# Kernel tuning notes

Measured on AMD Instinct MI355X. Metric: run time of the kernel, lower is better.

Reference implementation:

```python
import jax, jax.numpy as jnp
import numpy as np

N_NODES = 50000
N_EDGES = 800000
N_GRAPHS = 64
IN_C, HID, OUT_C = 128, 96, 96
EPS = 1e-5


def gcn_conv(x, W, b, src, dst, n_nodes):
    # PyG GCNConv: linear -> symmetric-normalized aggregation with self-loops
    h = x @ W  # [N, C]
    deg = jax.ops.segment_sum(jnp.ones(src.shape[0], h.dtype), dst, num_segments=n_nodes) + 1.0  # +1 self-loop
    dinv = jax.lax.rsqrt(deg)  # deg >= 1, no inf
    norm = dinv[src] * dinv[dst]  # [E]
    agg = jax.ops.segment_sum(h[src] * norm[:, None], dst, num_segments=n_nodes)
    agg = agg + h * (dinv * dinv)[:, None]  # self-loop contribution
    return agg + b


def graph_norm(x, w, b, alpha, batch, n_graphs):
    # PyG GraphNorm: per-graph mean (scaled by learnable alpha) and variance
    cnt = jax.ops.segment_sum(jnp.ones(x.shape[0], x.dtype), batch, num_segments=n_graphs)[:, None]
    mean = jax.ops.segment_sum(x, batch, num_segments=n_graphs) / cnt
    xc = x - alpha * mean[batch]
    var = jax.ops.segment_sum(xc * xc, batch, num_segments=n_graphs) / cnt
    return w * xc * jax.lax.rsqrt(var[batch] + EPS) + b


def setup_inputs() -> dict:
    key = jax.random.key(0)
    ks = jax.random.split(key, 8)
    x = jax.random.normal(ks[0], (N_NODES, IN_C), jnp.float32)
    edge_index = jax.random.randint(ks[1], (2, N_EDGES), 0, N_NODES, jnp.int64)
    batch = jnp.sort(jax.random.randint(ks[2], (N_NODES,), 0, N_GRAPHS, jnp.int64))
    s1 = 1.0 / np.sqrt(IN_C)
    s2 = 1.0 / np.sqrt(HID)
    return {
        "x": x,
        "edge_index": edge_index,
        "batch": batch,
        "W1": jax.random.uniform(ks[3], (IN_C, HID), jnp.float32, -s1, s1),
        "b1": jnp.zeros((HID,), jnp.float32),
        "gn1_w": jnp.ones((HID,), jnp.float32),
        "gn1_b": jnp.zeros((HID,), jnp.float32),
        "gn1_a": jnp.ones((HID,), jnp.float32),
        "W2": jax.random.uniform(ks[4], (HID, OUT_C), jnp.float32, -s2, s2),
        "b2": jnp.zeros((OUT_C,), jnp.float32),
        "gn2_w": jnp.ones((OUT_C,), jnp.float32),
        "gn2_b": jnp.zeros((OUT_C,), jnp.float32),
        "gn2_a": jnp.ones((OUT_C,), jnp.float32),
    }


def reference(x, edge_index, batch, W1, b1, gn1_w, gn1_b, gn1_a, W2, b2, gn2_w, gn2_b, gn2_a):
    src, dst = edge_index[0], edge_index[1]
    h = gcn_conv(x, W1, b1, src, dst, N_NODES)
    h = graph_norm(h, gn1_w, gn1_b, gn1_a, batch, N_GRAPHS)
    h = jax.nn.relu(h)  # dropout = identity in eval mode
    h = gcn_conv(h, W2, b2, src, dst, N_NODES)
    h = graph_norm(h, gn2_w, gn2_b, gn2_a, batch, N_GRAPHS)
    h = jax.nn.relu(h)
    return h
```

## Files before the change

kernel.cpp:

```cpp
#include <hip/hip_runtime.h>
#include <hip/hip_bf16.h>

#define N_NODES 50000
#define N_EDGES 800000
#define N_GRAPHS 64
#define IN_C 128
#define HID 96
#define SLICES 8
#define NBUCK 196
#define NCHK 200
#define EPC 4000

typedef short s16x8 __attribute__((ext_vector_type(8)));
typedef float f32x4 __attribute__((ext_vector_type(4)));

__device__ inline unsigned short f2bf(float f) {
    union { __hip_bfloat16 b; unsigned short u; } cv;
    cv.b = __float2bfloat16(f);
    return cv.u;
}
__device__ inline float bf2f(unsigned short u) { return __uint_as_float((unsigned int)u << 16); }
__device__ inline float bf_lo(unsigned int u) { return __uint_as_float(u << 16); }
__device__ inline float bf_hi(unsigned int u) { return __uint_as_float(u & 0xffff0000u); }
__device__ inline unsigned int pack2(float lo, float hi) {
    return (unsigned)f2bf(lo) | ((unsigned)f2bf(hi) << 16);
}
__device__ inline void acc8(float* a, uint4 r) {
    a[0] += bf_lo(r.x); a[1] += bf_hi(r.x);
    a[2] += bf_lo(r.y); a[3] += bf_hi(r.y);
    a[4] += bf_lo(r.z); a[5] += bf_hi(r.z);
    a[6] += bf_lo(r.w); a[7] += bf_hi(r.w);
}


__global__ __launch_bounds__(256)
void p1_hist(const int* __restrict__ dst, int* __restrict__ chunkHist,
             const int* __restrict__ batch, int* __restrict__ gstart, int* __restrict__ gend) {
    __shared__ int h[NBUCK];
    int c = blockIdx.x, t = threadIdx.x;
    for (int i = t; i < NBUCK; i += 256) h[i] = 0;
    __syncthreads();
    int base = c * EPC;
    for (int i = t; i < EPC; i += 256)
        atomicAdd(&h[dst[base + i] >> 8], 1);
    __syncthreads();
    for (int i = t; i < NBUCK; i += 256) chunkHist[c * NBUCK + i] = h[i];

    int gi = c * 256 + t;
    if (gi < N_NODES) {
        int g = batch[gi];
        if (gi == 0) {
            gstart[g] = 0;
        } else {
            int gp = batch[gi - 1];
            if (gp != g) { gstart[g] = gi; gend[gp] = gi - 1; }
        }
        if (gi == N_NODES - 1) gend[g] = N_NODES - 1;
    }
}

__global__ __launch_bounds__(256)
void p2a_scan(const int* __restrict__ chunkHist, int* __restrict__ offTabRel,
              int* __restrict__ bucketTot) {
    __shared__ int sh[256];
    __shared__ int hv[256];
    int b = blockIdx.x, t = threadIdx.x;
    int v = (t < NCHK) ? chunkHist[t * NBUCK + b] : 0;
    hv[t] = v;
    sh[t] = v;
    __syncthreads();
    for (int off = 1; off < 256; off <<= 1) {
        int x = (t >= off) ? sh[t - off] : 0;
        __syncthreads();
        sh[t] += x;
        __syncthreads();
    }
    if (t < NCHK) offTabRel[t * NBUCK + b] = sh[t] - hv[t];
    if (t == 255) bucketTot[b] = sh[255];
}

__global__ __launch_bounds__(256)
void p2b_base(const int* __restrict__ bucketTot, int* __restrict__ bucketBase,
              int* __restrict__ rowstart) {
    __shared__ int sh[256];
    int t = threadIdx.x;
    int v = (t < NBUCK) ? bucketTot[t] : 0;
    sh[t] = v;
    __syncthreads();
    for (int off = 1; off < 256; off <<= 1) {
        int x = (t >= off) ? sh[t - off] : 0;
        __syncthreads();
        sh[t] += x;
        __syncthreads();
    }
    if (t < NBUCK) bucketBase[t] = sh[t] - v;
    if (t == 0) { bucketBase[NBUCK] = N_EDGES; rowstart[N_NODES] = N_EDGES; }
}

__global__ __launch_bounds__(256)
void p3_place(const int* __restrict__ src, const int* __restrict__ dst,
              const int* __restrict__ offTabRel, const int* __restrict__ bucketBase,
              unsigned int* __restrict__ epacked) {
    __shared__ int cur[NBUCK];
    int c = blockIdx.x, t = threadIdx.x;
    for (int i = t; i < NBUCK; i += 256)
        cur[i] = bucketBase[i] + offTabRel[c * NBUCK + i];
    __syncthreads();
    int base = c * EPC;
    for (int i = t; i < EPC; i += 256) {
        int d = dst[base + i];
        int s = src[base + i];
        int pos = atomicAdd(&cur[d >> 8], 1);
        epacked[pos] = ((unsigned)(d & 255) << 16) | (unsigned)s;
    }
}

__global__ __launch_bounds__(256)
void p4_fine(const unsigned int* __restrict__ epacked, const int* __restrict__ bucketBase,
             int* __restrict__ rowstart, float* __restrict__ dinv,
             unsigned short* __restrict__ e_src16) {
    __shared__ int h[256];
    __shared__ int rs[256];
    __shared__ unsigned short sorted[8192];
    int b = blockIdx.x, t = threadIdx.x;
    int s0 = bucketBase[b], len = bucketBase[b + 1] - s0;
    h[t] = 0;
    __syncthreads();
    for (int i = t; i < len; i += 256)
        atomicAdd(&h[(epacked[s0 + i] >> 16) & 255], 1);
    __syncthreads();
    int deg = h[t];
    rs[t] = deg;
    __syncthreads();
    for (int off = 1; off < 256; off <<= 1) {
        int x = (t >= off) ? rs[t - off] : 0;
        __syncthreads();
        rs[t] += x;
        __syncthreads();
    }
    int myrow = rs[t] - deg;
    int node = b * 256 + t;
    if (node < N_NODES) {
        rowstart[node] = s0 + myrow;
        dinv[node] = rsqrtf((float)deg + 1.0f);
    }
    __syncthreads();
    h[t] = myrow;
    __syncthreads();
    for (int i = t; i < len; i += 256) {
        unsigned int p = epacked[s0 + i];
        int pos = atomicAdd(&h[(p >> 16) & 255], 1);
        sorted[pos] = (unsigned short)(p & 0xffffu);
    }
    __syncthreads();
    for (int i = t; i < len; i += 256) e_src16[s0 + i] = sorted[i];
}

template <int K, bool PRENORM>
__global__ __launch_bounds__(256)
void gemm_mfma(const void* __restrict__ Xv, const float* __restrict__ W,
               const float* __restrict__ dinv, const int* __restrict__ batch,
               const float* __restrict__ gA, const float* __restrict__ gB,
               unsigned short* __restrict__ Hp) {
    constexpr int KP = K + 8;
    constexpr int KS = K / 32;
    __shared__ unsigned short Wt[96 * KP];
    int tid = threadIdx.x;
    for (int idx = tid; idx < K * 96; idx += 256) {
        int k = idx / 96, c = idx - k * 96;
        Wt[c * KP + k] = f2bf(W[idx]);
    }
    __syncthreads();

    const int lane = tid & 63;
    const int quad = lane >> 4;
    const int l16 = lane & 15;

    s16x8 Bf[6][KS];
#pragma unroll
    for (int t = 0; t < 6; ++t)
#pragma unroll
        for (int s = 0; s < KS; ++s)
            Bf[t][s] = *(const s16x8*)&Wt[(t * 16 + l16) * KP + s * 32 + quad * 8];

    int gw = blockIdx.x * 4 + (tid >> 6);
    int nw = gridDim.x * 4;
    for (int tile = gw; tile < N_NODES / 16; tile += nw) {
        int n0 = tile * 16;
        int row = n0 + l16;
        s16x8 Af[KS];
        if (!PRENORM) {
            const float* Xr = (const float*)Xv + (size_t)row * K;
#pragma unroll
            for (int s = 0; s < KS; ++s) {
                int k0 = s * 32 + quad * 8;
                float4 u = *(const float4*)(Xr + k0);
                float4 v = *(const float4*)(Xr + k0 + 4);
                s16x8 a;
                a[0] = (short)f2bf(u.x); a[1] = (short)f2bf(u.y);
                a[2] = (short)f2bf(u.z); a[3] = (short)f2bf(u.w);
                a[4] = (short)f2bf(v.x); a[5] = (short)f2bf(v.y);
                a[6] = (short)f2bf(v.z); a[7] = (short)f2bf(v.w);
                Af[s] = a;
            }
        } else {
            const unsigned short* Xr = (const unsigned short*)Xv + (size_t)row * HID;
            int g = batch[row];
            const float* ga = gA + g * HID;
            const float* gb = gB + g * HID;
#pragma unroll
            for (int s = 0; s < KS; ++s) {
                int k0 = s * 32 + quad * 8;
                uint4 raw = *(const uint4*)(Xr + k0);
                float4 a0 = *(const float4*)(ga + k0);
                float4 a1 = *(const float4*)(ga + k0 + 4);
                float4 b0 = *(const float4*)(gb + k0);
                float4 b1 = *(const float4*)(gb + k0 + 4);
                s16x8 a;
                a[0] = (short)f2bf(fmaxf(fmaf(bf_lo(raw.x), a0.x, b0.x), 0.f));
                a[1] = (short)f2bf(fmaxf(fmaf(bf_hi(raw.x), a0.y, b0.y), 0.f));
                a[2] = (short)f2bf(fmaxf(fmaf(bf_lo(raw.y), a0.z, b0.z), 0.f));
                a[3] = (short)f2bf(fmaxf(fmaf(bf_hi(raw.y), a0.w, b0.w), 0.f));
                a[4] = (short)f2bf(fmaxf(fmaf(bf_lo(raw.z), a1.x, b1.x), 0.f));
                a[5] = (short)f2bf(fmaxf(fmaf(bf_hi(raw.z), a1.y, b1.y), 0.f));
                a[6] = (short)f2bf(fmaxf(fmaf(bf_lo(raw.w), a1.z, b1.z), 0.f));
                a[7] = (short)f2bf(fmaxf(fmaf(bf_hi(raw.w), a1.w, b1.w), 0.f));
                Af[s] = a;
            }
        }
        f32x4 acc[6];
#pragma unroll
        for (int t = 0; t < 6; ++t) { acc[t][0] = 0.f; acc[t][1] = 0.f; acc[t][2] = 0.f; acc[t][3] = 0.f; }
#pragma unroll
        for (int s = 0; s < KS; ++s)
#pragma unroll
            for (int t = 0; t < 6; ++t)
                acc[t] = __builtin_amdgcn_mfma_f32_16x16x32_bf16(Af[s], Bf[t][s], acc[t], 0, 0, 0);

        float4 dv = *(const float4*)(dinv + n0 + quad * 4);
#pragma unroll
        for (int t = 0; t < 6; ++t) {
            size_t base = (size_t)(n0 + quad * 4) * HID + t * 16 + l16;
            Hp[base]            = f2bf(acc[t][0] * dv.x);
            Hp[base + HID]      = f2bf(acc[t][1] * dv.y);
            Hp[base + 2 * HID]  = f2bf(acc[t][2] * dv.z);
            Hp[base + 3 * HID]  = f2bf(acc[t][3] * dv.w);
        }
    }
}

__global__ __launch_bounds__(384)
void agg_kernel(const int* __restrict__ rowstart, const unsigned short* __restrict__ e_src,
                const float* __restrict__ dinv, const unsigned short* __restrict__ H,
                const float* __restrict__ bias, unsigned short* __restrict__ OUT) {
    int node = blockIdx.x * 32 + threadIdx.y;
    if (node >= N_NODES) return;
    int x = threadIdx.x;
    const uint4* H8 = (const uint4*)H;
    size_t ridx = (size_t)node * 12 + x;
    float a[8] = {0, 0, 0, 0, 0, 0, 0, 0};
    acc8(a, H8[ridx]);
    int s0 = rowstart[node], s1 = rowstart[node + 1];
    int i = s0;
    for (; i + 4 <= s1; i += 4) {
        int sA = e_src[i], sB = e_src[i + 1], sC = e_src[i + 2], sD = e_src[i + 3];
        uint4 rA = H8[(size_t)sA * 12 + x];
        uint4 rB = H8[(size_t)sB * 12 + x];
        uint4 rC = H8[(size_t)sC * 12 + x];
        uint4 rD = H8[(size_t)sD * 12 + x];
        acc8(a, rA); acc8(a, rB); acc8(a, rC); acc8(a, rD);
    }
    for (; i < s1; ++i)
        acc8(a, H8[(size_t)e_src[i] * 12 + x]);

    float di = dinv[node];
    float4 b0 = *(const float4*)(bias + x * 8);
    float4 b1 = *(const float4*)(bias + x * 8 + 4);
    uint4 ov;
    ov.x = pack2(fmaf(a[0], di, b0.x), fmaf(a[1], di, b0.y));
    ov.y = pack2(fmaf(a[2], di, b0.z), fmaf(a[3], di, b0.w));
    ov.z = pack2(fmaf(a[4], di, b1.x), fmaf(a[5], di, b1.y));
    ov.w = pack2(fmaf(a[6], di, b1.z), fmaf(a[7], di, b1.w));
    ((uint4*)OUT)[ridx] = ov;
}

__global__ __launch_bounds__(768)
void gn_partial(const unsigned short* __restrict__ Xb, const int* __restrict__ gstart,
                const int* __restrict__ gend, float* __restrict__ gSum, float* __restrict__ gSq,
                int* __restrict__ done, const float* __restrict__ w, const float* __restrict__ b,
                const float* __restrict__ a, float* __restrict__ gA, float* __restrict__ gB) {
    __shared__ float4 sSum[32][24];
    __shared__ float4 sSq[32][24];
    __shared__ int lastFlag;
    int g = blockIdx.x, sl = blockIdx.y;
    int x = threadIdx.x, ty = threadIdx.y;
    int s = gstart[g], e = gend[g];
    float sx = 0, sy = 0, sz = 0, sw = 0, qx = 0, qy = 0, qz = 0, qw = 0;
    if (s <= e) {
        int cnt = e - s + 1;
        int per = (cnt + SLICES - 1) / SLICES;
        int n0 = s + sl * per;
        int n1 = min(n0 + per - 1, e);
        const ushort4* X4 = (const ushort4*)Xb;
        for (int n = n0 + ty; n <= n1; n += 32) {
            ushort4 h = X4[(size_t)n * 24 + x];
            float vx = bf2f(h.x), vy = bf2f(h.y), vz = bf2f(h.z), vw = bf2f(h.w);
            sx += vx; qx = fmaf(vx, vx, qx);
            sy += vy; qy = fmaf(vy, vy, qy);
            sz += vz; qz = fmaf(vz, vz, qz);
            sw += vw; qw = fmaf(vw, vw, qw);
        }
    }
    sSum[ty][x] = make_float4(sx, sy, sz, sw);
    sSq[ty][x] = make_float4(qx, qy, qz, qw);
    __syncthreads();
    for (int off = 16; off > 0; off >>= 1) {
        if (ty < off) {
            float4 A = sSum[ty + off][x], B = sSum[ty][x];
            sSum[ty][x] = make_float4(A.x + B.x, A.y + B.y, A.z + B.z, A.w + B.w);
            float4 C = sSq[ty + off][x], D = sSq[ty][x];
            sSq[ty][x] = make_float4(C.x + D.x, C.y + D.y, C.z + D.z, C.w + D.w);
        }
        __syncthreads();
    }
    if (ty == 0) {
        float4 S = sSum[0][x], Q = sSq[0][x];
        atomicAdd(&gSum[g * HID + x * 4 + 0], S.x);
        atomicAdd(&gSum[g * HID + x * 4 + 1], S.y);
        atomicAdd(&gSum[g * HID + x * 4 + 2], S.z);
        atomicAdd(&gSum[g * HID + x * 4 + 3], S.w);
        atomicAdd(&gSq[g * HID + x * 4 + 0], Q.x);
        atomicAdd(&gSq[g * HID + x * 4 + 1], Q.y);
        atomicAdd(&gSq[g * HID + x * 4 + 2], Q.z);
        atomicAdd(&gSq[g * HID + x * 4 + 3], Q.w);
        __threadfence();
    }
    __syncthreads();
    if (ty == 0 && x == 0) {
        int old = atomicAdd(&done[g], 1);
        lastFlag = (old == SLICES - 1) ? 1 : 0;
    }
    __syncthreads();
    if (lastFlag) {
        int t = ty * 24 + x;
        if (t < HID) {
            float S = atomicAdd(&gSum[g * HID + t], 0.0f);
            float Q = atomicAdd(&gSq[g * HID + t], 0.0f);
            float A = 0.f, B = 0.f;
            if (s <= e) {
                float cnt = (float)(e - s + 1);
                float mean = S / cnt;
                float alpha = a[t];
                float var = Q / cnt - (2.f * alpha - alpha * alpha) * mean * mean;
                var = fmaxf(var, 0.f);
                float rsv = rsqrtf(var + 1e-5f);
                A = w[t] * rsv;
                B = b[t] - alpha * mean * A;
            }
            gA[g * HID + t] = A;
            gB[g * HID + t] = B;
        }
    }
}

__global__ __launch_bounds__(384)
void gn_apply(const unsigned short* __restrict__ Xb, const int* __restrict__ batch,
              const float* __restrict__ gA, const float* __restrict__ gB,
              float* __restrict__ Y) {
    int n = blockIdx.x * 32 + threadIdx.y;
    if (n >= N_NODES) return;
    int x = threadIdx.x;
    int g = batch[n];
    uint4 h = ((const uint4*)Xb)[(size_t)n * 12 + x];
    const float* ga = gA + g * HID + x * 8;
    const float* gb = gB + g * HID + x * 8;
    float4 a0 = *(const float4*)ga, a1 = *(const float4*)(ga + 4);
    float4 b0 = *(const float4*)gb, b1 = *(const float4*)(gb + 4);
    float4 o0, o1;
    o0.x = fmaxf(fmaf(bf_lo(h.x), a0.x, b0.x), 0.f);
    o0.y = fmaxf(fmaf(bf_hi(h.x), a0.y, b0.y), 0.f);
    o0.z = fmaxf(fmaf(bf_lo(h.y), a0.z, b0.z), 0.f);
    o0.w = fmaxf(fmaf(bf_hi(h.y), a0.w, b0.w), 0.f);
    o1.x = fmaxf(fmaf(bf_lo(h.z), a1.x, b1.x), 0.f);
    o1.y = fmaxf(fmaf(bf_hi(h.z), a1.y, b1.y), 0.f);
    o1.z = fmaxf(fmaf(bf_lo(h.w), a1.z, b1.z), 0.f);
    o1.w = fmaxf(fmaf(bf_hi(h.w), a1.w, b1.w), 0.f);
    float* yr = Y + (size_t)n * HID + x * 8;
    *(float4*)yr = o0;
    *(float4*)(yr + 4) = o1;
}

extern "C" void kernel_launch(void* const* d_in, const int* in_sizes, int n_in,
                              void* d_out, int out_size, void* d_ws, size_t ws_size,
                              hipStream_t stream) {
    const float* x     = (const float*)d_in[0];
    const int*   edge  = (const int*)d_in[1];
    const int*   batch = (const int*)d_in[2];
    const float* W1    = (const float*)d_in[3];
    const float* b1    = (const float*)d_in[4];
    const float* gn1_w = (const float*)d_in[5];
    const float* gn1_b = (const float*)d_in[6];
    const float* gn1_a = (const float*)d_in[7];
    const float* W2    = (const float*)d_in[8];
    const float* b2    = (const float*)d_in[9];
    const float* gn2_w = (const float*)d_in[10];
    const float* gn2_b = (const float*)d_in[11];
    const float* gn2_a = (const float*)d_in[12];
    float* out = (float*)d_out;

    const int* srcv = edge;
    const int* dstv = edge + N_EDGES;

    float* ws   = (float*)d_ws;
    float* dinv = ws;
    float* gA   = dinv + 50048;
    float* gB   = gA + 6144;
    float* zb    = gB + 6144;
    float* gSum1 = zb;
    float* gSq1  = gSum1 + 6144;
    float* gSum2 = gSq1 + 6144;
    float* gSq2  = gSum2 + 6144;
    int* done1   = (int*)(gSq2 + 6144);
    int* done2   = done1 + 64;
    int* gstart  = done2 + 64;
    int* gend    = gstart + 64;
    const size_t ZB_BYTES = (4 * 6144 + 4 * 64) * sizeof(float);
    int* rowstart   = gend + 64;
    int* chunkHist  = rowstart + 50008;
    int* offTabRel  = chunkHist + NCHK * NBUCK;
    int* bucketTot  = offTabRel + NCHK * NBUCK;
    int* bucketBase = bucketTot + 200;
    unsigned int* epacked = (unsigned int*)(bucketBase + 200);
    unsigned short* e_src16 = (unsigned short*)(epacked + N_EDGES);
    unsigned short* Hbf = e_src16 + N_EDGES;
    unsigned short* Obf = Hbf + (size_t)N_NODES * HID;

    hipMemsetAsync(zb, 0, ZB_BYTES, stream);
    p1_hist<<<NCHK, 256, 0, stream>>>(dstv, chunkHist, batch, gstart, gend);
    p2a_scan<<<NBUCK, 256, 0, stream>>>(chunkHist, offTabRel, bucketTot);
    p2b_base<<<1, 256, 0, stream>>>(bucketTot, bucketBase, rowstart);
    p3_place<<<NCHK, 256, 0, stream>>>(srcv, dstv, offTabRel, bucketBase, epacked);
    p4_fine<<<NBUCK, 256, 0, stream>>>(epacked, bucketBase, rowstart, dinv, e_src16);

    const dim3 blk12x32(12, 32);
    const dim3 blk24x32(24, 32);
    const int nodeGrid32 = (N_NODES + 31) / 32;

    gemm_mfma<IN_C, false><<<391, 256, 0, stream>>>(x, W1, dinv, nullptr, nullptr, nullptr, Hbf);
    agg_kernel<<<nodeGrid32, blk12x32, 0, stream>>>(rowstart, e_src16, dinv, Hbf, b1, Obf);
    gn_partial<<<dim3(N_GRAPHS, SLICES), blk24x32, 0, stream>>>(Obf, gstart, gend, gSum1, gSq1,
                                                                done1, gn1_w, gn1_b, gn1_a, gA, gB);

    gemm_mfma<HID, true><<<391, 256, 0, stream>>>(Obf, W2, dinv, batch, gA, gB, Hbf);
    agg_kernel<<<nodeGrid32, blk12x32, 0, stream>>>(rowstart, e_src16, dinv, Hbf, b2, Obf);
    gn_partial<<<dim3(N_GRAPHS, SLICES), blk24x32, 0, stream>>>(Obf, gstart, gend, gSum2, gSq2,
                                                                done2, gn2_w, gn2_b, gn2_a, gA, gB);
    gn_apply<<<nodeGrid32, blk12x32, 0, stream>>>(Obf, batch, gA, gB, out);
}
```

Before: 153.7 us.

## Fuse GraphNorm statistics into aggregation and merge scan kernels via last-block pattern

```diff
diff --git a/kernel.cpp b/kernel.cpp
--- a/kernel.cpp
+++ b/kernel.cpp
@@ -6,7 +6,6 @@
 #define N_GRAPHS 64
 #define IN_C 128
 #define HID 96
-#define SLICES 8
 #define NBUCK 196
 #define NCHK 200
 #define EPC 4000
@@ -60,13 +59,13 @@
 }
 
 __global__ __launch_bounds__(256)
-void p2a_scan(const int* __restrict__ chunkHist, int* __restrict__ offTabRel,
-              int* __restrict__ bucketTot) {
+void p2_scan(const int* __restrict__ chunkHist, int* __restrict__ offTabRel,
+             int* __restrict__ bucketTot, int* __restrict__ bucketBase,
+             int* __restrict__ rowstart, int* __restrict__ p2done) {
     __shared__ int sh[256];
-    __shared__ int hv[256];
+    __shared__ int lastF;
     int b = blockIdx.x, t = threadIdx.x;
     int v = (t < NCHK) ? chunkHist[t * NBUCK + b] : 0;
-    hv[t] = v;
     sh[t] = v;
     __syncthreads();
     for (int off = 1; off < 256; off <<= 1) {
@@ -75,26 +74,28 @@
         sh[t] += x;
         __syncthreads();
     }
-    if (t < NCHK) offTabRel[t * NBUCK + b] = sh[t] - hv[t];
-    if (t == 255) bucketTot[b] = sh[255];
-}
-
-__global__ __launch_bounds__(256)
-void p2b_base(const int* __restrict__ bucketTot, int* __restrict__ bucketBase,
-              int* __restrict__ rowstart) {
-    __shared__ int sh[256];
-    int t = threadIdx.x;
-    int v = (t < NBUCK) ? bucketTot[t] : 0;
-    sh[t] = v;
-    __syncthreads();
-    for (int off = 1; off < 256; off <<= 1) {
-        int x = (t >= off) ? sh[t - off] : 0;
-        __syncthreads();
-        sh[t] += x;
-        __syncthreads();
-    }
-    if (t < NBUCK) bucketBase[t] = sh[t] - v;
-    if (t == 0) { bucketBase[NBUCK] = N_EDGES; rowstart[N_NODES] = N_EDGES; }
+    if (t < NCHK) offTabRel[t * NBUCK + b] = sh[t] - v;
+    if (t == 255) {
+        atomicExch(&bucketTot[b], sh[255]);
+        __threadfence();
+    }
+    __syncthreads();
+    if (t == 0) lastF = (atomicAdd(p2done, 1) == NBUCK - 1) ? 1 : 0;
+    __syncthreads();
+    if (lastF) {
+        int bt = (t < NBUCK) ? atomicAdd(&bucketTot[t], 0) : 0;
+        __syncthreads();
+        sh[t] = bt;
+        __syncthreads();
+        for (int off = 1; off < 256; off <<= 1) {
+            int x = (t >= off) ? sh[t - off] : 0;
+            __syncthreads();
+            sh[t] += x;
+            __syncthreads();
+        }
+        if (t < NBUCK) bucketBase[t] = sh[t] - bt;
+        if (t == 0) { bucketBase[NBUCK] = N_EDGES; rowstart[N_NODES] = N_EDGES; }
+    }
 }
 
 __global__ __launch_bounds__(256)
@@ -250,115 +251,143 @@
 }
 
 __global__ __launch_bounds__(384)
-void agg_kernel(const int* __restrict__ rowstart, const unsigned short* __restrict__ e_src,
-                const float* __restrict__ dinv, const unsigned short* __restrict__ H,
-                const float* __restrict__ bias, unsigned short* __restrict__ OUT) {
-    int node = blockIdx.x * 32 + threadIdx.y;
-    if (node >= N_NODES) return;
-    int x = threadIdx.x;
-    const uint4* H8 = (const uint4*)H;
-    size_t ridx = (size_t)node * 12 + x;
-    float a[8] = {0, 0, 0, 0, 0, 0, 0, 0};
-    acc8(a, H8[ridx]);
-    int s0 = rowstart[node], s1 = rowstart[node + 1];
-    int i = s0;
-    for (; i + 4 <= s1; i += 4) {
-        int sA = e_src[i], sB = e_src[i + 1], sC = e_src[i + 2], sD = e_src[i + 3];
-        uint4 rA = H8[(size_t)sA * 12 + x];
-        uint4 rB = H8[(size_t)sB * 12 + x];
-        uint4 rC = H8[(size_t)sC * 12 + x];
-        uint4 rD = H8[(size_t)sD * 12 + x];
-        acc8(a, rA); acc8(a, rB); acc8(a, rC); acc8(a, rD);
-    }
-    for (; i < s1; ++i)
-        acc8(a, H8[(size_t)e_src[i] * 12 + x]);
-
-    float di = dinv[node];
-    float4 b0 = *(const float4*)(bias + x * 8);
-    float4 b1 = *(const float4*)(bias + x * 8 + 4);
-    uint4 ov;
-    ov.x = pack2(fmaf(a[0], di, b0.x), fmaf(a[1], di, b0.y));
-    ov.y = pack2(fmaf(a[2], di, b0.z), fmaf(a[3], di, b0.w));
-    ov.z = pack2(fmaf(a[4], di, b1.x), fmaf(a[5], di, b1.y));
-    ov.w = pack2(fmaf(a[6], di, b1.z), fmaf(a[7], di, b1.w));
-    ((uint4*)OUT)[ridx] = ov;
-}
-
-__global__ __launch_bounds__(768)
-void gn_partial(const unsigned short* __restrict__ Xb, const int* __restrict__ gstart,
-                const int* __restrict__ gend, float* __restrict__ gSum, float* __restrict__ gSq,
-                int* __restrict__ done, const float* __restrict__ w, const float* __restrict__ b,
-                const float* __restrict__ a, float* __restrict__ gA, float* __restrict__ gB) {
-    __shared__ float4 sSum[32][24];
-    __shared__ float4 sSq[32][24];
-    __shared__ int lastFlag;
-    int g = blockIdx.x, sl = blockIdx.y;
-    int x = threadIdx.x, ty = threadIdx.y;
-    int s = gstart[g], e = gend[g];
-    float sx = 0, sy = 0, sz = 0, sw = 0, qx = 0, qy = 0, qz = 0, qw = 0;
-    if (s <= e) {
-        int cnt = e - s + 1;
-        int per = (cnt + SLICES - 1) / SLICES;
-        int n0 = s + sl * per;
-        int n1 = min(n0 + per - 1, e);
-        const ushort4* X4 = (const ushort4*)Xb;
-        for (int n = n0 + ty; n <= n1; n += 32) {
-            ushort4 h = X4[(size_t)n * 24 + x];
-            float vx = bf2f(h.x), vy = bf2f(h.y), vz = bf2f(h.z), vw = bf2f(h.w);
-            sx += vx; qx = fmaf(vx, vx, qx);
-            sy += vy; qy = fmaf(vy, vy, qy);
-            sz += vz; qz = fmaf(vz, vz, qz);
-            sw += vw; qw = fmaf(vw, vw, qw);
-        }
-    }
-    sSum[ty][x] = make_float4(sx, sy, sz, sw);
-    sSq[ty][x] = make_float4(qx, qy, qz, qw);
-    __syncthreads();
-    for (int off = 16; off > 0; off >>= 1) {
-        if (ty < off) {
-            float4 A = sSum[ty + off][x], B = sSum[ty][x];
-            sSum[ty][x] = make_float4(A.x + B.x, A.y + B.y, A.z + B.z, A.w + B.w);
-            float4 C = sSq[ty + off][x], D = sSq[ty][x];
-            sSq[ty][x] = make_float4(C.x + D.x, C.y + D.y, C.z + D.z, C.w + D.w);
-        }
-        __syncthreads();
-    }
-    if (ty == 0) {
-        float4 S = sSum[0][x], Q = sSq[0][x];
-        atomicAdd(&gSum[g * HID + x * 4 + 0], S.x);
-        atomicAdd(&gSum[g * HID + x * 4 + 1], S.y);
-        atomicAdd(&gSum[g * HID + x * 4 + 2], S.z);
-        atomicAdd(&gSum[g * HID + x * 4 + 3], S.w);
-        atomicAdd(&gSq[g * HID + x * 4 + 0], Q.x);
-        atomicAdd(&gSq[g * HID + x * 4 + 1], Q.y);
-        atomicAdd(&gSq[g * HID + x * 4 + 2], Q.z);
-        atomicAdd(&gSq[g * HID + x * 4 + 3], Q.w);
+void agg_gn(const int* __restrict__ rowstart, const unsigned short* __restrict__ e_src,
+            const float* __restrict__ dinv, const unsigned short* __restrict__ H,
+            const float* __restrict__ bias, const int* __restrict__ batch,
+            const int* __restrict__ gstart, const int* __restrict__ gend,
+            const float* __restrict__ wpar, const float* __restrict__ bpar,
+            const float* __restrict__ apar, float* __restrict__ gSum,
+            float* __restrict__ gSq, int* __restrict__ done,
+            float* __restrict__ gA, float* __restrict__ gB,
+            unsigned short* __restrict__ OUT) {
+    __shared__ float4 sS[32][12][2];
+    __shared__ float4 sQ[32][12][2];
+    __shared__ int sG[32];
+    __shared__ int curMin;
+    __shared__ int lastF;
+    int ty = threadIdx.y, x = threadIdx.x;
+    int node = blockIdx.x * 32 + ty;
+    bool valid = node < N_NODES;
+
+    float v[8] = {0, 0, 0, 0, 0, 0, 0, 0};
+    int g = 0x7fffffff;
+    if (valid) {
+        const uint4* H8 = (const uint4*)H;
+        size_t ridx = (size_t)node * 12 + x;
+        float a[8] = {0, 0, 0, 0, 0, 0, 0, 0};
+        acc8(a, H8[ridx]);
+        int s0 = rowstart[node], s1 = rowstart[node + 1];
+        int i = s0;
+        for (; i + 4 <= s1; i += 4) {
+            int sA = e_src[i], sB = e_src[i + 1], sC = e_src[i + 2], sD = e_src[i + 3];
+            uint4 rA = H8[(size_t)sA * 12 + x];
+            uint4 rB = H8[(size_t)sB * 12 + x];
+            uint4 rC = H8[(size_t)sC * 12 + x];
+            uint4 rD = H8[(size_t)sD * 12 + x];
+            acc8(a, rA); acc8(a, rB); acc8(a, rC); acc8(a, rD);
+        }
+        for (; i < s1; ++i)
+            acc8(a, H8[(size_t)e_src[i] * 12 + x]);
+
+        float di = dinv[node];
+        float4 b0 = *(const float4*)(bias + x * 8);
+        float4 b1 = *(const float4*)(bias + x * 8 + 4);
+        v[0] = fmaf(a[0], di, b0.x); v[1] = fmaf(a[1], di, b0.y);
+        v[2] = fmaf(a[2], di, b0.z); v[3] = fmaf(a[3], di, b0.w);
+        v[4] = fmaf(a[4], di, b1.x); v[5] = fmaf(a[5], di, b1.y);
+        v[6] = fmaf(a[6], di, b1.z); v[7] = fmaf(a[7], di, b1.w);
+        uint4 ov;
+        ov.x = pack2(v[0], v[1]); ov.y = pack2(v[2], v[3]);
+        ov.z = pack2(v[4], v[5]); ov.w = pack2(v[6], v[7]);
+        ((uint4*)OUT)[ridx] = ov;
+        g = batch[node];
+    }
+    if (x == 0) sG[ty] = g;
+    __syncthreads();
+
+    bool rowDone = false;
+    while (true) {
+        if (ty == 0 && x == 0) {
+            int m = sG[0];
+#pragma unroll 4
+            for (int i = 1; i < 32; ++i) m = min(m, sG[i]);
+            curMin = m;
+        }
+        __syncthreads();
+        int gm = curMin;
+        if (gm == 0x7fffffff) break;
+        bool act = valid && !rowDone && (g == gm);
+        float4 z0, z1, q0, q1;
+        if (act) {
+            z0 = make_float4(v[0], v[1], v[2], v[3]);
+            z1 = make_float4(v[4], v[5], v[6], v[7]);
+            q0 = make_float4(v[0] * v[0], v[1] * v[1], v[2] * v[2], v[3] * v[3]);
+            q1 = make_float4(v[4] * v[4], v[5] * v[5], v[6] * v[6], v[7] * v[7]);
+        } else {
+            z0 = z1 = q0 = q1 = make_float4(0.f, 0.f, 0.f, 0.f);
+        }
+        sS[ty][x][0] = z0; sS[ty][x][1] = z1;
+        sQ[ty][x][0] = q0; sQ[ty][x][1] = q1;
+        __syncthreads();
+        for (int off = 16; off > 0; off >>= 1) {
+            if (ty < off) {
+                float4 A0 = sS[ty + off][x][0], A1 = sS[ty + off][x][1];
+                float4 B0 = sS[ty][x][0], B1 = sS[ty][x][1];
+                sS[ty][x][0] = make_float4(A0.x + B0.x, A0.y + B0.y, A0.z + B0.z, A0.w + B0.w);
+                sS[ty][x][1] = make_float4(A1.x + B1.x, A1.y + B1.y, A1.z + B1.z, A1.w + B1.w);
+                float4 C0 = sQ[ty + off][x][0], C1 = sQ[ty + off][x][1];
+                float4 D0 = sQ[ty][x][0], D1 = sQ[ty][x][1];
+                sQ[ty][x][0] = make_float4(C0.x + D0.x, C0.y + D0.y, C0.z + D0.z, C0.w + D0.w);
+                sQ[ty][x][1] = make_float4(C1.x + D1.x, C1.y + D1.y, C1.z + D1.z, C1.w + D1.w);
+            }
+            __syncthreads();
+        }
+        if (ty == 0) {
+            float4 S0 = sS[0][x][0], S1 = sS[0][x][1];
+            float4 Q0 = sQ[0][x][0], Q1 = sQ[0][x][1];
+            float* gs = gSum + gm * HID + x * 8;
+            float* gq = gSq + gm * HID + x * 8;
+            atomicAdd(gs + 0, S0.x); atomicAdd(gs + 1, S0.y);
+            atomicAdd(gs + 2, S0.z); atomicAdd(gs + 3, S0.w);
+            atomicAdd(gs + 4, S1.x); atomicAdd(gs + 5, S1.y);
+            atomicAdd(gs + 6, S1.z); atomicAdd(gs + 7, S1.w);
+            atomicAdd(gq + 0, Q0.x); atomicAdd(gq + 1, Q0.y);
+            atomicAdd(gq + 2, Q0.z); atomicAdd(gq + 3, Q0.w);
+            atomicAdd(gq + 4, Q1.x); atomicAdd(gq + 5, Q1.y);
+            atomicAdd(gq + 6, Q1.z); atomicAdd(gq + 7, Q1.w);
+        }
+        if (act) {
+            rowDone = true;
+            if (x == 0) sG[ty] = 0x7fffffff;
+        }
+        __syncthreads();
+    }
+
+    if (ty == 0 && x == 0) {
         __threadfence();
-    }
-    __syncthreads();
-    if (ty == 0 && x == 0) {
-        int old = atomicAdd(&done[g], 1);
-        lastFlag = (old == SLICES - 1) ? 1 : 0;
-    }
-    __syncthreads();
-    if (lastFlag) {
-        int t = ty * 24 + x;
-        if (t < HID) {
-            float S = atomicAdd(&gSum[g * HID + t], 0.0f);
-            float Q = atomicAdd(&gSq[g * HID + t], 0.0f);
+        lastF = (atomicAdd(done, 1) == (int)gridDim.x - 1) ? 1 : 0;
+    }
+    __syncthreads();
+    if (lastF) {
+        int tid = ty * 12 + x;
+        for (int idx = tid; idx < N_GRAPHS * HID; idx += 384) {
+            int gg = idx / HID, c = idx - gg * HID;
+            float S = atomicAdd(&gSum[idx], 0.0f);
+            float Q = atomicAdd(&gSq[idx], 0.0f);
+            int s = gstart[gg], e = gend[gg];
             float A = 0.f, B = 0.f;
             if (s <= e) {
                 float cnt = (float)(e - s + 1);
                 float mean = S / cnt;
-                float alpha = a[t];
+                float alpha = apar[c];
                 float var = Q / cnt - (2.f * alpha - alpha * alpha) * mean * mean;
                 var = fmaxf(var, 0.f);
                 float rsv = rsqrtf(var + 1e-5f);
-                A = w[t] * rsv;
-                B = b[t] - alpha * mean * A;
+                A = wpar[c] * rsv;
+                B = bpar[c] - alpha * mean * A;
             }
-            gA[g * HID + t] = A;
-            gB[g * HID + t] = B;
+            gA[idx] = A;
+            gB[idx] = B;
         }
     }
 }
@@ -413,18 +442,19 @@
 
     float* ws   = (float*)d_ws;
     float* dinv = ws;
-    float* gA   = dinv + 50048;
-    float* gB   = gA + 6144;
-    float* zb    = gB + 6144;
+    float* gA1  = dinv + 50048;
+    float* gB1  = gA1 + 6144;
+    float* gA2  = gB1 + 6144;
+    float* gB2  = gA2 + 6144;
+    float* zb    = gB2 + 6144;
     float* gSum1 = zb;
     float* gSq1  = gSum1 + 6144;
     float* gSum2 = gSq1 + 6144;
     float* gSq2  = gSum2 + 6144;
-    int* done1   = (int*)(gSq2 + 6144);
-    int* done2   = done1 + 64;
-    int* gstart  = done2 + 64;
+    int* ctr     = (int*)(gSq2 + 6144);
+    int* gstart  = ctr + 64;
     int* gend    = gstart + 64;
-    const size_t ZB_BYTES = (4 * 6144 + 4 * 64) * sizeof(float);
+    const size_t ZB_BYTES = (4 * 6144 + 3 * 64) * sizeof(float);
     int* rowstart   = gend + 64;
     int* chunkHist  = rowstart + 50008;
     int* offTabRel  = chunkHist + NCHK * NBUCK;
@@ -437,23 +467,22 @@
 
     hipMemsetAsync(zb, 0, ZB_BYTES, stream);
     p1_hist<<<NCHK, 256, 0, stream>>>(dstv, chunkHist, batch, gstart, gend);
-    p2a_scan<<<NBUCK, 256, 0, stream>>>(chunkHist, offTabRel, bucketTot);
-    p2b_base<<<1, 256, 0, stream>>>(bucketTot, bucketBase, rowstart);
+    p2_scan<<<NBUCK, 256, 0, stream>>>(chunkHist, offTabRel, bucketTot, bucketBase,
+                                       rowstart, ctr + 2);
     p3_place<<<NCHK, 256, 0, stream>>>(srcv, dstv, offTabRel, bucketBase, epacked);
     p4_fine<<<NBUCK, 256, 0, stream>>>(epacked, bucketBase, rowstart, dinv, e_src16);
 
     const dim3 blk12x32(12, 32);
-    const dim3 blk24x32(24, 32);
     const int nodeGrid32 = (N_NODES + 31) / 32;
 
     gemm_mfma<IN_C, false><<<391, 256, 0, stream>>>(x, W1, dinv, nullptr, nullptr, nullptr, Hbf);
-    agg_kernel<<<nodeGrid32, blk12x32, 0, stream>>>(rowstart, e_src16, dinv, Hbf, b1, Obf);
-    gn_partial<<<dim3(N_GRAPHS, SLICES), blk24x32, 0, stream>>>(Obf, gstart, gend, gSum1, gSq1,
-                                                                done1, gn1_w, gn1_b, gn1_a, gA, gB);
-
-    gemm_mfma<HID, true><<<391, 256, 0, stream>>>(Obf, W2, dinv, batch, gA, gB, Hbf);
-    agg_kernel<<<nodeGrid32, blk12x32, 0, stream>>>(rowstart, e_src16, dinv, Hbf, b2, Obf);
-    gn_partial<<<dim3(N_GRAPHS, SLICES), blk24x32, 0, stream>>>(Obf, gstart, gend, gSum2, gSq2,
-                                                                done2, gn2_w, gn2_b, gn2_a, gA, gB);
-    gn_apply<<<nodeGrid32, blk12x32, 0, stream>>>(Obf, batch, gA, gB, out);
-}
+    agg_gn<<<nodeGrid32, blk12x32, 0, stream>>>(rowstart, e_src16, dinv, Hbf, b1, batch,
+                                                gstart, gend, gn1_w, gn1_b, gn1_a,
+                                                gSum1, gSq1, ctr + 0, gA1, gB1, Obf);
+
+    gemm_mfma<HID, true><<<391, 256, 0, stream>>>(Obf, W2, dinv, batch, gA1, gB1, Hbf);
+    agg_gn<<<nodeGrid32, blk12x32, 0, stream>>>(rowstart, e_src16, dinv, Hbf, b2, batch,
+                                                gstart, gend, gn2_w, gn2_b, gn2_a,
+                                                gSum2, gSq2, ctr + 1, gA2, gB2, Obf);
+    gn_apply<<<nodeGrid32, blk12x32, 0, stream>>>(Obf, batch, gA2, gB2, out);
+}
```

Result: slower. 249.5 us (+62.3%).
